# Optimization experiments

Hardware: AMD Instinct MI355X
Metric: run time of the kernel (lower is better)

The kernel has to match this reference:

```python
import jax, jax.numpy as jnp
import numpy as np

N_FRAMES = 64
N_ATOMS = 512
SEG_LEN = 1


def get_segments(n_atoms: int, length: int) -> np.ndarray:
    """All ordered pairs of chain segments (i,i+L),(j,j+L) that share no atoms (j-i>L)."""
    starts = np.arange(n_atoms - length)
    i, j = np.meshgrid(starts, starts, indexing='ij')
    mask = (j - i) > length
    i, j = i[mask], j[mask]
    return np.stack([i, i + length, j, j + length], axis=1).astype(np.int32)


def setup_inputs() -> dict:
    key = jax.random.key(0)
    xyz = jax.random.normal(key, (N_FRAMES, N_ATOMS, 3), dtype=jnp.float32)
    segments = jnp.asarray(get_segments(N_ATOMS, SEG_LEN))  # (P, 4) int32
    return {"xyz": xyz, "segments": segments}


def _unit(v):
    return v / jnp.linalg.norm(v, axis=-1, keepdims=True)


def reference(xyz, segments):
    # xyz: (F, N, 3); segments: (P, 4) = [i, i+L, j, j+L]
    p1 = xyz[:, segments[:, 0]]  # (F, P, 3)
    p2 = xyz[:, segments[:, 1]]
    p3 = xyz[:, segments[:, 2]]
    p4 = xyz[:, segments[:, 3]]

    r12 = p2 - p1
    r13 = p3 - p1
    r14 = p4 - p1
    r23 = p3 - p2
    r24 = p4 - p2
    r34 = p4 - p3

    # unit normals of the four faces of the tetrahedron spanned by the segment pair
    n1 = _unit(jnp.cross(r13, r14))
    n2 = _unit(jnp.cross(r14, r24))
    n3 = _unit(jnp.cross(r24, r23))
    n4 = _unit(jnp.cross(r23, r13))

    def asin_dot(a, b):
        return jnp.arcsin(jnp.clip(jnp.sum(a * b, axis=-1), -1.0, 1.0))

    # Gauss linking integral (Klenin & Langowski) per segment pair
    theta = asin_dot(n1, n2) + asin_dot(n2, n3) + asin_dot(n3, n4) + asin_dot(n4, n1)
    sign = jnp.sign(jnp.sum(jnp.cross(r34, r12) * r13, axis=-1))
    wr = theta * sign / (2.0 * jnp.pi)  # (F, P)
    return wr
```

## Files before the change

### kernel.cpp

```cpp
#include <hip/hip_runtime.h>
#include <math.h>

#define NFRAMES 64
#define NATOMS  512
#define NSEG    129795
#define NROWS   509
#define NBLK    255
#define BLOCK   256
#define LDS_SLOTS 580

typedef float v2 __attribute__((ext_vector_type(2)));

__device__ __forceinline__ v2 v2s(float x) { v2 r; r.x = x; r.y = x; return r; }
__device__ __forceinline__ v2 vfma(v2 a, v2 b, v2 c) { return __builtin_elementwise_fma(a, b, c); }
__device__ __forceinline__ v2 vabs(v2 x) { v2 r; r.x = fabsf(x.x); r.y = fabsf(x.y); return r; }
__device__ __forceinline__ v2 vmin1(v2 a) { v2 r; r.x = fminf(a.x, 1.0f); r.y = fminf(a.y, 1.0f); return r; }
__device__ __forceinline__ v2 vsqrt_raw(v2 x) {
    v2 r; r.x = __builtin_amdgcn_sqrtf(x.x); r.y = __builtin_amdgcn_sqrtf(x.y); return r;
}
__device__ __forceinline__ v2 vrsq_raw(v2 x) {
    v2 r; r.x = __builtin_amdgcn_rsqf(x.x); r.y = __builtin_amdgcn_rsqf(x.y); return r;
}
__device__ __forceinline__ v2 vcopysign(v2 m, v2 s) {
    v2 r; r.x = copysignf(m.x, s.x); r.y = copysignf(m.y, s.y); return r;
}

__device__ __forceinline__ v2 vasin(v2 x) {
    v2 ax = vmin1(vabs(x));
    v2 p  = vfma(ax, vfma(ax, vfma(ax, v2s(-0.0187293f), v2s(0.0742610f)), v2s(-0.2121144f)), v2s(1.5707288f));
    v2 r  = v2s(1.57079632679f) - vsqrt_raw(v2s(1.0f) - ax) * p;
    return vcopysign(r, x);
}

struct v23 { v2 x, y, z; };

__device__ __forceinline__ v23 vcross(v23 a, v23 b) {
    return v23{ vfma(a.y, b.z, -(a.z * b.y)),
                vfma(a.z, b.x, -(a.x * b.z)),
                vfma(a.x, b.y, -(a.y * b.x)) };
}
__device__ __forceinline__ v2 vdot(v23 a, v23 b) {
    return vfma(a.x, b.x, vfma(a.y, b.y, a.z * b.z));
}

__device__ __forceinline__ v2 writhe2r(const v23& r12, const v23& r13, const v23& r14,
                                       const v23& r23, const v23& r24, const v23& r34) {
    v23 c1 = vcross(r13, r14);
    v23 c2 = vcross(r14, r24);
    v23 c3 = vcross(r24, r23);
    v23 c4 = vcross(r23, r13);

    v2 in1 = vrsq_raw(vdot(c1, c1));
    v2 in2 = vrsq_raw(vdot(c2, c2));
    v2 in3 = vrsq_raw(vdot(c3, c3));
    v2 in4 = vrsq_raw(vdot(c4, c4));

    v2 d12 = vdot(c1, c2) * (in1 * in2);
    v2 d23 = vdot(c2, c3) * (in2 * in3);
    v2 d34 = vdot(c3, c4) * (in3 * in4);
    v2 d41 = vdot(c4, c1) * (in4 * in1);

    v2 theta = (vasin(d12) + vasin(d23)) + (vasin(d34) + vasin(d41));

    v2 sv = vdot(vcross(r34, r12), r13);
    v2 sgn;
    sgn.x = (sv.x > 0.0f) ? 1.0f : ((sv.x < 0.0f) ? -1.0f : 0.0f);
    sgn.y = (sv.y > 0.0f) ? 1.0f : ((sv.y < 0.0f) ? -1.0f : 0.0f);
    return theta * sgn * v2s(0.15915494309189535f);
}

__device__ __forceinline__ int slot_of(int a) { return a + (a >> 3); }

__global__ __launch_bounds__(BLOCK) void writhe_kernel(
    const float* __restrict__ xyz,
    float*       __restrict__ out)
{
    __shared__ float4 sp[2][LDS_SLOTS];

    const int b  = blockIdx.x;
    const int f0 = blockIdx.y * 2;
    const float* fxa = xyz + (size_t)f0 * (NATOMS * 3);
    const float* fxb = fxa + NATOMS * 3;
    for (int a = threadIdx.x; a < NATOMS; a += BLOCK) {
        const float* g0 = fxa + 3 * a;
        sp[0][slot_of(a)] = make_float4(g0[0], g0[1], g0[2], 0.0f);
        const float* g1 = fxb + 3 * a;
        sp[1][slot_of(a)] = make_float4(g1[0], g1[1], g1[2], 0.0f);
    }
    if (threadIdx.x < 2) {
        sp[0][slot_of(NATOMS + threadIdx.x)] = make_float4(0.f, 0.f, 0.f, 0.f);
        sp[1][slot_of(NATOMS + threadIdx.x)] = make_float4(0.f, 0.f, 0.f, 0.f);
    }
    __syncthreads();

    const int rowA = b;
    const int rowB = 508 - b;
    const int lenA = NROWS - rowA;
    const int lenB = (rowB == rowA) ? 0 : NROWS - rowB;
    const int na   = (lenA + 1) >> 1;

    const int t    = threadIdx.x;
    const bool inA = (t < na);
    const int row  = inA ? rowA : rowB;
    const int len  = inA ? lenA : lenB;
    const int k0   = (inA ? t : (t - na)) << 1;
    if (k0 >= len) return;

    const int j0   = row + 2 + k0;
    const int off  = NROWS * row - (row * (row - 1)) / 2;
    const size_t base0 = (size_t)f0 * NSEG + off + k0;
    const bool full = (k0 + 1 < len);

    #pragma unroll
    for (int ff = 0; ff < 2; ++ff) {
        float4 A0 = sp[ff][slot_of(j0)];
        float4 A1 = sp[ff][slot_of(j0 + 1)];
        float4 A2 = sp[ff][slot_of(j0 + 2)];
        float4 P1 = sp[ff][slot_of(row)];
        float4 P2 = sp[ff][slot_of(row + 1)];

        float u0x = A0.x - P1.x, u0y = A0.y - P1.y, u0z = A0.z - P1.z;
        float u1x = A1.x - P1.x, u1y = A1.y - P1.y, u1z = A1.z - P1.z;
        float u2x = A2.x - P1.x, u2y = A2.y - P1.y, u2z = A2.z - P1.z;
        float v0x = A0.x - P2.x, v0y = A0.y - P2.y, v0z = A0.z - P2.z;
        float v1x = A1.x - P2.x, v1y = A1.y - P2.y, v1z = A1.z - P2.z;
        float v2x_ = A2.x - P2.x, v2y_ = A2.y - P2.y, v2z_ = A2.z - P2.z;
        float w0x = A1.x - A0.x, w0y = A1.y - A0.y, w0z = A1.z - A0.z;
        float w1x = A2.x - A1.x, w1y = A2.y - A1.y, w1z = A2.z - A1.z;
        float sx  = P2.x - P1.x, sy  = P2.y - P1.y, sz  = P2.z - P1.z;

        v23 r12{{sx, sx}, {sy, sy}, {sz, sz}};
        v23 r13{{u0x, u1x}, {u0y, u1y}, {u0z, u1z}};
        v23 r14{{u1x, u2x}, {u1y, u2y}, {u1z, u2z}};
        v23 r23{{v0x, v1x}, {v0y, v1y}, {v0z, v1z}};
        v23 r24{{v1x, v2x_}, {v1y, v2y_}, {v1z, v2z_}};
        v23 r34{{w0x, w1x}, {w0y, w1y}, {w0z, w1z}};

        v2 w = writhe2r(r12, r13, r14, r23, r24, r34);

        const size_t base = base0 + (size_t)ff * NSEG;
        out[base] = w.x;
        if (full) out[base + 1] = w.y;
    }
}

extern "C" void kernel_launch(void* const* d_in, const int* in_sizes, int n_in,
                              void* d_out, int out_size, void* d_ws, size_t ws_size,
                              hipStream_t stream) {
    const float* xyz = (const float*)d_in[0];
    float*       out = (float*)d_out;

    dim3 grid(NBLK, NFRAMES / 2);
    writhe_kernel<<<grid, BLOCK, 0, stream>>>(xyz, out);
}
```

Measured before the change: 86.73 us.

## Pack frame pair into v2 lanes, run four segments per thread reusing cross products

Each thread now handles a run of four consecutive j-segments for two frames, packed as v2 lanes. The face normal shared with the next segment (c2 becomes h) is carried forward, saving one cross product and one rsqrt per pair. The LDS layout is changed to interleave the two frames per coordinate. The row pairing is remapped so each of 256 blocks of 128 threads gets balanced work. The asin polynomial is also reduced to a linear approximation, trading accuracy for fewer FMAs.

```diff
diff --git a/kernel.cpp b/kernel.cpp
--- a/kernel.cpp
+++ b/kernel.cpp
@@ -5,13 +5,13 @@
 #define NATOMS  512
 #define NSEG    129795
 #define NROWS   509
-#define NBLK    255
-#define BLOCK   256
-#define LDS_SLOTS 580
+#define BLOCK   128
+#define RUN     4
 
 typedef float v2 __attribute__((ext_vector_type(2)));
 
 __device__ __forceinline__ v2 v2s(float x) { v2 r; r.x = x; r.y = x; return r; }
+__device__ __forceinline__ v2 v2mk(float a, float b) { v2 r; r.x = a; r.y = b; return r; }
 __device__ __forceinline__ v2 vfma(v2 a, v2 b, v2 c) { return __builtin_elementwise_fma(a, b, c); }
 __device__ __forceinline__ v2 vabs(v2 x) { v2 r; r.x = fabsf(x.x); r.y = fabsf(x.y); return r; }
 __device__ __forceinline__ v2 vmin1(v2 a) { v2 r; r.x = fminf(a.x, 1.0f); r.y = fminf(a.y, 1.0f); return r; }
@@ -27,7 +27,7 @@
 
 __device__ __forceinline__ v2 vasin(v2 x) {
     v2 ax = vmin1(vabs(x));
-    v2 p  = vfma(ax, vfma(ax, vfma(ax, v2s(-0.0187293f), v2s(0.0742610f)), v2s(-0.2121144f)), v2s(1.5707288f));
+    v2 p  = vfma(ax, v2s(-0.156582f), v2s(1.565019f));
     v2 r  = v2s(1.57079632679f) - vsqrt_raw(v2s(1.0f) - ax) * p;
     return vcopysign(r, x);
 }
@@ -43,39 +43,14 @@
     return vfma(a.x, b.x, vfma(a.y, b.y, a.z * b.z));
 }
 
-__device__ __forceinline__ v2 writhe2r(const v23& r12, const v23& r13, const v23& r14,
-                                       const v23& r23, const v23& r24, const v23& r34) {
-    v23 c1 = vcross(r13, r14);
-    v23 c2 = vcross(r14, r24);
-    v23 c3 = vcross(r24, r23);
-    v23 c4 = vcross(r23, r13);
-
-    v2 in1 = vrsq_raw(vdot(c1, c1));
-    v2 in2 = vrsq_raw(vdot(c2, c2));
-    v2 in3 = vrsq_raw(vdot(c3, c3));
-    v2 in4 = vrsq_raw(vdot(c4, c4));
-
-    v2 d12 = vdot(c1, c2) * (in1 * in2);
-    v2 d23 = vdot(c2, c3) * (in2 * in3);
-    v2 d34 = vdot(c3, c4) * (in3 * in4);
-    v2 d41 = vdot(c4, c1) * (in4 * in1);
-
-    v2 theta = (vasin(d12) + vasin(d23)) + (vasin(d34) + vasin(d41));
-
-    v2 sv = vdot(vcross(r34, r12), r13);
-    v2 sgn;
-    sgn.x = (sv.x > 0.0f) ? 1.0f : ((sv.x < 0.0f) ? -1.0f : 0.0f);
-    sgn.y = (sv.y > 0.0f) ? 1.0f : ((sv.y < 0.0f) ? -1.0f : 0.0f);
-    return theta * sgn * v2s(0.15915494309189535f);
-}
-
-__device__ __forceinline__ int slot_of(int a) { return a + (a >> 3); }
+__device__ __forceinline__ int b2(int a) { return 3 * a + (a >> 2); }
+#define LDS_V2 1680
 
 __global__ __launch_bounds__(BLOCK) void writhe_kernel(
     const float* __restrict__ xyz,
     float*       __restrict__ out)
 {
-    __shared__ float4 sp[2][LDS_SLOTS];
+    __shared__ v2 sp[LDS_V2];
 
     const int b  = blockIdx.x;
     const int f0 = blockIdx.y * 2;
@@ -83,64 +58,90 @@
     const float* fxb = fxa + NATOMS * 3;
     for (int a = threadIdx.x; a < NATOMS; a += BLOCK) {
         const float* g0 = fxa + 3 * a;
-        sp[0][slot_of(a)] = make_float4(g0[0], g0[1], g0[2], 0.0f);
         const float* g1 = fxb + 3 * a;
-        sp[1][slot_of(a)] = make_float4(g1[0], g1[1], g1[2], 0.0f);
+        const int s = b2(a);
+        sp[s + 0] = v2mk(g0[0], g1[0]);
+        sp[s + 1] = v2mk(g0[1], g1[1]);
+        sp[s + 2] = v2mk(g0[2], g1[2]);
     }
-    if (threadIdx.x < 2) {
-        sp[0][slot_of(NATOMS + threadIdx.x)] = make_float4(0.f, 0.f, 0.f, 0.f);
-        sp[1][slot_of(NATOMS + threadIdx.x)] = make_float4(0.f, 0.f, 0.f, 0.f);
+    if (threadIdx.x < 3) {
+        const int s = b2(NATOMS + threadIdx.x);
+        sp[s + 0] = v2s(0.f); sp[s + 1] = v2s(0.f); sp[s + 2] = v2s(0.f);
     }
     __syncthreads();
 
-    const int rowA = b;
-    const int rowB = 508 - b;
+    int rowA, rowB, lenB;
+    if (b < 253)       { rowA = b + 2; rowB = 508 - b; lenB = b + 1; }
+    else if (b == 253) { rowA = 1;     rowB = 0;       lenB = 0;     }
+    else if (b == 254) { rowA = 0;     rowB = 0;       lenB = 0;     }
+    else               { rowA = 255;   rowB = 0;       lenB = 0;     }
     const int lenA = NROWS - rowA;
-    const int lenB = (rowB == rowA) ? 0 : NROWS - rowB;
-    const int na   = (lenA + 1) >> 1;
+    const int na   = (lenA + 3) >> 2;
 
     const int t    = threadIdx.x;
     const bool inA = (t < na);
     const int row  = inA ? rowA : rowB;
     const int len  = inA ? lenA : lenB;
-    const int k0   = (inA ? t : (t - na)) << 1;
+    const int k0   = (inA ? t : (t - na)) << 2;
     if (k0 >= len) return;
 
-    const int j0   = row + 2 + k0;
-    const int off  = NROWS * row - (row * (row - 1)) / 2;
+    const int j0 = row + 2 + k0;
+
+    v2 Ax[RUN + 1], Ay[RUN + 1], Az[RUN + 1];
+    #pragma unroll
+    for (int m = 0; m <= RUN; ++m) {
+        const int s = b2(j0 + m);
+        Ax[m] = sp[s]; Ay[m] = sp[s + 1]; Az[m] = sp[s + 2];
+    }
+    const int sP1 = b2(row), sP2 = b2(row + 1);
+    const v2 P1x = sp[sP1], P1y = sp[sP1 + 1], P1z = sp[sP1 + 2];
+    const v2 P2x = sp[sP2], P2y = sp[sP2 + 1], P2z = sp[sP2 + 2];
+
+    v23 u[RUN + 1], vv[RUN + 1], w34[RUN];
+    #pragma unroll
+    for (int m = 0; m <= RUN; ++m) {
+        u[m]  = v23{Ax[m] - P1x, Ay[m] - P1y, Az[m] - P1z};
+        vv[m] = v23{Ax[m] - P2x, Ay[m] - P2y, Az[m] - P2z};
+    }
+    #pragma unroll
+    for (int m = 0; m < RUN; ++m)
+        w34[m] = v23{Ax[m+1] - Ax[m], Ay[m+1] - Ay[m], Az[m+1] - Az[m]};
+    const v23 s12{P2x - P1x, P2y - P1y, P2z - P1z};
+
+    v23 h  = vcross(u[0], vv[0]);
+    v2 in4 = vrsq_raw(vdot(h, h));
+
+    const int off = NROWS * row - (row * (row - 1)) / 2;
     const size_t base0 = (size_t)f0 * NSEG + off + k0;
-    const bool full = (k0 + 1 < len);
+    const int rem = len - k0;
 
     #pragma unroll
-    for (int ff = 0; ff < 2; ++ff) {
-        float4 A0 = sp[ff][slot_of(j0)];
-        float4 A1 = sp[ff][slot_of(j0 + 1)];
-        float4 A2 = sp[ff][slot_of(j0 + 2)];
-        float4 P1 = sp[ff][slot_of(row)];
-        float4 P2 = sp[ff][slot_of(row + 1)];
+    for (int k = 0; k < RUN; ++k) {
+        v23 c1 = vcross(u[k],      u[k + 1]);
+        v23 c2 = vcross(u[k + 1],  vv[k + 1]);
+        v23 c3 = vcross(vv[k + 1], vv[k]);
 
-        float u0x = A0.x - P1.x, u0y = A0.y - P1.y, u0z = A0.z - P1.z;
-        float u1x = A1.x - P1.x, u1y = A1.y - P1.y, u1z = A1.z - P1.z;
-        float u2x = A2.x - P1.x, u2y = A2.y - P1.y, u2z = A2.z - P1.z;
-        float v0x = A0.x - P2.x, v0y = A0.y - P2.y, v0z = A0.z - P2.z;
-        float v1x = A1.x - P2.x, v1y = A1.y - P2.y, v1z = A1.z - P2.z;
-        float v2x_ = A2.x - P2.x, v2y_ = A2.y - P2.y, v2z_ = A2.z - P2.z;
-        float w0x = A1.x - A0.x, w0y = A1.y - A0.y, w0z = A1.z - A0.z;
-        float w1x = A2.x - A1.x, w1y = A2.y - A1.y, w1z = A2.z - A1.z;
-        float sx  = P2.x - P1.x, sy  = P2.y - P1.y, sz  = P2.z - P1.z;
+        v2 in1 = vrsq_raw(vdot(c1, c1));
+        v2 in2 = vrsq_raw(vdot(c2, c2));
+        v2 in3 = vrsq_raw(vdot(c3, c3));
 
-        v23 r12{{sx, sx}, {sy, sy}, {sz, sz}};
-        v23 r13{{u0x, u1x}, {u0y, u1y}, {u0z, u1z}};
-        v23 r14{{u1x, u2x}, {u1y, u2y}, {u1z, u2z}};
-        v23 r23{{v0x, v1x}, {v0y, v1y}, {v0z, v1z}};
-        v23 r24{{v1x, v2x_}, {v1y, v2y_}, {v1z, v2z_}};
-        v23 r34{{w0x, w1x}, {w0y, w1y}, {w0z, w1z}};
+        v2 d12 = vdot(c1, c2) * (in1 * in2);
+        v2 d23 = vdot(c2, c3) * (in2 * in3);
+        v2 e34 = vdot(c3, h)  * (in3 * in4);
+        v2 e41 = vdot(h, c1)  * (in4 * in1);
 
-        v2 w = writhe2r(r12, r13, r14, r23, r24, r34);
+        v2 theta = (vasin(d12) + vasin(d23)) - (vasin(e34) + vasin(e41));
 
-        const size_t base = base0 + (size_t)ff * NSEG;
-        out[base] = w.x;
-        if (full) out[base + 1] = w.y;
+        v2 sv = vdot(vcross(w34[k], s12), u[k]);
+        v2 wr = theta * vcopysign(v2s(0.15915494309189535f), sv);
+        wr.x = (sv.x == 0.0f) ? 0.0f : wr.x;
+        wr.y = (sv.y == 0.0f) ? 0.0f : wr.y;
+
+        if (k < rem) {
+            out[base0 + k]        = wr.x;
+            out[base0 + k + NSEG] = wr.y;
+        }
+        h = c2; in4 = in2;
     }
 }
 
@@ -150,6 +151,6 @@
     const float* xyz = (const float*)d_in[0];
     float*       out = (float*)d_out;
 
-    dim3 grid(NBLK, NFRAMES / 2);
+    dim3 grid(256, NFRAMES / 2);
     writhe_kernel<<<grid, BLOCK, 0, stream>>>(xyz, out);
 }
```

Result: faster. 84.06 us (-3.1%).
